# Kernel tuning notes

Hardware: AMD Instinct MI355X
Metric: run time of the kernel (lower is better)

## Reference

```python
import jax, jax.numpy as jnp
import numpy as np

EPS = 1e-5

def layer_norm(x, g, b):
    mu = jnp.mean(x, axis=-1, keepdims=True)
    var = jnp.var(x, axis=-1, keepdims=True)
    return (x - mu) * jax.lax.rsqrt(var + EPS) * g + b

def setup_inputs() -> dict:
    key = jax.random.key(0)
    ks = jax.random.split(key, 8)
    B, N, C, H = 4, 1024, 1024, 16
    Dh = C * 4
    std = 0.02
    return {
        "x": jax.random.normal(ks[0], (B, N, C), dtype=jnp.float32),
        "qkv_w": jax.random.normal(ks[1], (3 * C, C), dtype=jnp.float32) * std,
        "proj_w": jax.random.normal(ks[2], (C, C), dtype=jnp.float32) * std,
        "proj_b": jnp.zeros((C,), dtype=jnp.float32),
        "fc1_w": jax.random.normal(ks[3], (Dh, C), dtype=jnp.float32) * std,
        "fc1_b": jnp.zeros((Dh,), dtype=jnp.float32),
        "fc2_w": jax.random.normal(ks[4], (C, Dh), dtype=jnp.float32) * std,
        "fc2_b": jnp.zeros((C,), dtype=jnp.float32),
        "ln1_g": jnp.ones((C,), dtype=jnp.float32),
        "ln1_b": jnp.zeros((C,), dtype=jnp.float32),
        "ln2_g": jnp.ones((C,), dtype=jnp.float32),
        "ln2_b": jnp.zeros((C,), dtype=jnp.float32),
        "lnh_g": jnp.ones((Dh,), dtype=jnp.float32),
        "lnh_b": jnp.zeros((Dh,), dtype=jnp.float32),
    }

def reference(x, qkv_w, proj_w, proj_b, fc1_w, fc1_b, fc2_w, fc2_b,
              ln1_g, ln1_b, ln2_g, ln2_b, lnh_g, lnh_b):
    B, N, C = x.shape
    H = 16
    Dh = C // H
    scale = Dh ** (-0.5)

    # --- attention sublayer (pre-norm) ---
    h = layer_norm(x, ln1_g, ln1_b)
    qkv = (h @ qkv_w.T).reshape(B, N, 3, H, Dh).transpose(2, 0, 3, 1, 4)  # [3,B,H,N,Dh]
    q, k, v = qkv[0], qkv[1], qkv[2]
    attn = jnp.einsum('bhid,bhjd->bhij', q, k) * scale
    attn = jax.nn.softmax(attn, axis=-1)
    o = jnp.einsum('bhij,bhjd->bhid', attn, v)          # [B,H,N,Dh]
    o = o.transpose(0, 2, 1, 3).reshape(B, N, C)
    o = o @ proj_w.T + proj_b
    x = x + o

    # --- MLP sublayer (pre-norm, with LN on hidden per use_ln=True) ---
    h = layer_norm(x, ln2_g, ln2_b)
    u = jax.nn.gelu(h @ fc1_w.T + fc1_b, approximate=False)  # torch nn.GELU = erf form
    u = layer_norm(u, lnh_g, lnh_b)
    m = u @ fc2_w.T + fc2_b
    return x + m
```

## Files before the change

### kernel.cpp

```cpp
#include <hip/hip_runtime.h>
#include <hip/hip_bf16.h>
#include <math.h>


#define TOKENS 4096
#define CDIM   1024
#define HEADS  16
#define DHEAD  64
#define HID    4096

typedef __attribute__((ext_vector_type(4))) float  floatx4;
typedef __attribute__((ext_vector_type(8))) short  short8;

__device__ __forceinline__ void gl_lds16(const void* g, void* l)
{
    __builtin_amdgcn_global_load_lds(
        (const __attribute__((address_space(1))) unsigned int*)g,
        (__attribute__((address_space(3))) unsigned int*)l,
        16, 0, 0);
}

__global__ __launch_bounds__(256) void cvt_all(
    const float* __restrict__ s0, const float* __restrict__ s1,
    const float* __restrict__ s2, const float* __restrict__ s3,
    __hip_bfloat16* __restrict__ dst)
{
    long i = (long)blockIdx.x * 256 + threadIdx.x;
    const float* src;
    long base;
    if (i < 768l * 1024)       { src = s0; base = 0; }
    else if (i < 1792l * 1024) { src = s1; base = 768l * 1024; }
    else if (i < 2816l * 1024) { src = s2; base = 1792l * 1024; }
    else                       { src = s3; base = 2816l * 1024; }
    float4 v = ((const float4*)src)[i - base];
    __hip_bfloat16 t[4];
    t[0] = __float2bfloat16(v.x);
    t[1] = __float2bfloat16(v.y);
    t[2] = __float2bfloat16(v.z);
    t[3] = __float2bfloat16(v.w);
    *(uint2*)(dst + 4l * i) = *(uint2*)t;
}

__global__ __launch_bounds__(256) void ln_f32_kernel(
    const float* __restrict__ x, const float* __restrict__ g,
    const float* __restrict__ b, __hip_bfloat16* __restrict__ y, int C)
{
    int row = blockIdx.x;
    const float4* xr = (const float4*)(x + (long)row * C);
    uint2* yr = (uint2*)(y + (long)row * C);
    const int C4 = C >> 2;

    float s = 0.f, ss = 0.f;
    for (int i = threadIdx.x; i < C4; i += 256) {
        float4 v = xr[i];
        s  += v.x + v.y + v.z + v.w;
        ss += v.x * v.x + v.y * v.y + v.z * v.z + v.w * v.w;
    }
    #pragma unroll
    for (int d = 32; d; d >>= 1) {
        s  += __shfl_down(s, d);
        ss += __shfl_down(ss, d);
    }
    __shared__ float buf[4][2];
    int wid = threadIdx.x >> 6, lane = threadIdx.x & 63;
    if (lane == 0) { buf[wid][0] = s; buf[wid][1] = ss; }
    __syncthreads();
    if (threadIdx.x == 0) {
        s = buf[0][0] + buf[1][0] + buf[2][0] + buf[3][0];
        ss = buf[0][1] + buf[1][1] + buf[2][1] + buf[3][1];
        buf[0][0] = s; buf[0][1] = ss;
    }
    __syncthreads();
    s = buf[0][0]; ss = buf[0][1];

    float invC = 1.f / (float)C;
    float mu = s * invC;
    float var = ss * invC - mu * mu;
    float inv = rsqrtf(var + 1e-5f);
    const float4* gg = (const float4*)g;
    const float4* bb = (const float4*)b;
    for (int i = threadIdx.x; i < C4; i += 256) {
        float4 v = xr[i], gv = gg[i], bv = bb[i];
        __hip_bfloat16 t[4];
        t[0] = __float2bfloat16((v.x - mu) * inv * gv.x + bv.x);
        t[1] = __float2bfloat16((v.y - mu) * inv * gv.y + bv.y);
        t[2] = __float2bfloat16((v.z - mu) * inv * gv.z + bv.z);
        t[3] = __float2bfloat16((v.w - mu) * inv * gv.w + bv.w);
        yr[i] = *(uint2*)t;
    }
}

__global__ __launch_bounds__(256) void ln_bf16_kernel(
    const __hip_bfloat16* __restrict__ x, const float* __restrict__ g,
    const float* __restrict__ b, __hip_bfloat16* __restrict__ y, int C)
{
    int row = blockIdx.x;
    const uint4* xr = (const uint4*)(x + (long)row * C);
    uint4* yr = (uint4*)(y + (long)row * C);
    const int C8 = C >> 3;

    float s = 0.f, ss = 0.f;
    for (int i = threadIdx.x; i < C8; i += 256) {
        uint4 raw = xr[i];
        const __hip_bfloat16* p = (const __hip_bfloat16*)&raw;
        #pragma unroll
        for (int j = 0; j < 8; ++j) {
            float v = __bfloat162float(p[j]);
            s += v; ss += v * v;
        }
    }
    #pragma unroll
    for (int d = 32; d; d >>= 1) {
        s  += __shfl_down(s, d);
        ss += __shfl_down(ss, d);
    }
    __shared__ float buf[4][2];
    int wid = threadIdx.x >> 6, lane = threadIdx.x & 63;
    if (lane == 0) { buf[wid][0] = s; buf[wid][1] = ss; }
    __syncthreads();
    if (threadIdx.x == 0) {
        s = buf[0][0] + buf[1][0] + buf[2][0] + buf[3][0];
        ss = buf[0][1] + buf[1][1] + buf[2][1] + buf[3][1];
        buf[0][0] = s; buf[0][1] = ss;
    }
    __syncthreads();
    s = buf[0][0]; ss = buf[0][1];

    float invC = 1.f / (float)C;
    float mu = s * invC;
    float var = ss * invC - mu * mu;
    float inv = rsqrtf(var + 1e-5f);
    const float4* gg = (const float4*)g;
    const float4* bb = (const float4*)b;
    for (int i = threadIdx.x; i < C8; i += 256) {
        uint4 raw = xr[i];
        const __hip_bfloat16* p = (const __hip_bfloat16*)&raw;
        float4 g0 = gg[2 * i], g1 = gg[2 * i + 1];
        float4 b0 = bb[2 * i], b1 = bb[2 * i + 1];
        __hip_bfloat16 t[8];
        t[0] = __float2bfloat16((__bfloat162float(p[0]) - mu) * inv * g0.x + b0.x);
        t[1] = __float2bfloat16((__bfloat162float(p[1]) - mu) * inv * g0.y + b0.y);
        t[2] = __float2bfloat16((__bfloat162float(p[2]) - mu) * inv * g0.z + b0.z);
        t[3] = __float2bfloat16((__bfloat162float(p[3]) - mu) * inv * g0.w + b0.w);
        t[4] = __float2bfloat16((__bfloat162float(p[4]) - mu) * inv * g1.x + b1.x);
        t[5] = __float2bfloat16((__bfloat162float(p[5]) - mu) * inv * g1.y + b1.y);
        t[6] = __float2bfloat16((__bfloat162float(p[6]) - mu) * inv * g1.z + b1.z);
        t[7] = __float2bfloat16((__bfloat162float(p[7]) - mu) * inv * g1.w + b1.w);
        yr[i] = *(uint4*)t;
    }
}

__global__ __launch_bounds__(256, 3) void gemm_gl(
    const __hip_bfloat16* __restrict__ A,
    const __hip_bfloat16* __restrict__ W,
    const float* __restrict__ bias,
    void* __restrict__ Cout, int M, int N, int K, int mode)
{
    __shared__ __align__(16) __hip_bfloat16 Asl[128][64];
    __shared__ __align__(16) __hip_bfloat16 Bsl[128][64];

    int tid = threadIdx.x;
    int wave = tid >> 6, lane = tid & 63;

    int mt, nt;
    {
        int gx = gridDim.x, gy = gridDim.y;
        int lin = blockIdx.y * gx + blockIdx.x;
        int chunk = gy >> 3;
        int xcd = lin & 7, q = lin >> 3;
        mt = xcd * chunk + (q % chunk);
        nt = q / chunk;
    }
    int bm = mt * 128, bn = nt * 128;
    int wm = wave & 1, wn = wave >> 1;
    int fm = lane & 15, quad = lane >> 4;

    const int KS = K / gridDim.z;
    const long kz = (long)blockIdx.z * KS;
    const int nk = KS / 64;

    const int rsub = lane >> 3;
    const int csub = lane & 7;
    const __hip_bfloat16* gA[4];
    const __hip_bfloat16* gB[4];
    char* dA[4];
    char* dB[4];
    #pragma unroll
    for (int j = 0; j < 4; ++j) {
        int seg = wave * 4 + j;
        gA[j] = A + (long)(bm + seg * 8 + rsub) * K + kz + csub * 8;
        gB[j] = W + (long)(bn + seg * 8 + rsub) * K + kz + csub * 8;
        dA[j] = (char*)&Asl[0][0] + seg * 1024;
        dB[j] = (char*)&Bsl[0][0] + seg * 1024;
    }

    floatx4 acc[4][4] = {};

    for (int kt = 0; kt < nk; ++kt) {
        const long ko = (long)kt * 64;
        #pragma unroll
        for (int j = 0; j < 4; ++j) {
            gl_lds16(gA[j] + ko, dA[j]);
            gl_lds16(gB[j] + ko, dB[j]);
        }
        __syncthreads();

        #pragma unroll
        for (int kh = 0; kh < 2; ++kh) {
            short8 bq[4];
            #pragma unroll
            for (int j = 0; j < 4; ++j)
                bq[j] = *(const short8*)((const char*)&Bsl[0][0]
                        + (wn * 64 + j * 16 + fm) * 128 + kh * 64 + quad * 16);
            #pragma unroll
            for (int i = 0; i < 4; ++i) {
                short8 af = *(const short8*)((const char*)&Asl[0][0]
                        + (wm * 64 + i * 16 + fm) * 128 + kh * 64 + quad * 16);
                #pragma unroll
                for (int j = 0; j < 4; ++j)
                    acc[i][j] = __builtin_amdgcn_mfma_f32_16x16x32_bf16(
                        af, bq[j], acc[i][j], 0, 0, 0);
            }
        }
        __syncthreads();
    }

    int mbase = bm + wm * 64;
    int nbase = bn + wn * 64;
    if (mode == 2) {
        float* Cf = (float*)Cout;
        const bool addb = (blockIdx.z == 0);
        #pragma unroll
        for (int i = 0; i < 4; ++i) {
            #pragma unroll
            for (int j = 0; j < 4; ++j) {
                int ncol = nbase + j * 16 + fm;
                float bv = addb ? bias[ncol] : 0.f;
                #pragma unroll
                for (int r = 0; r < 4; ++r) {
                    int mrow = mbase + i * 16 + quad * 4 + r;
                    atomicAdd(&Cf[(long)mrow * N + ncol], acc[i][j][r] + bv);
                }
            }
        }
    } else {
        __hip_bfloat16* Cb = (__hip_bfloat16*)Cout;
        #pragma unroll
        for (int i = 0; i < 4; ++i) {
            #pragma unroll
            for (int j = 0; j < 4; ++j) {
                int ncol = nbase + j * 16 + fm;
                #pragma unroll
                for (int r = 0; r < 4; ++r) {
                    int mrow = mbase + i * 16 + quad * 4 + r;
                    float v = acc[i][j][r];
                    if (bias) v += bias[ncol];
                    if (mode == 1) {
                        float z = v * (1.5957691216f + 0.0713548162f * v * v);
                        v = v / (1.f + __expf(-z));
                    }
                    Cb[(long)mrow * N + ncol] = __float2bfloat16(v);
                }
            }
        }
    }
}

#define STR128 80
__global__ __launch_bounds__(256, 3) void gemm128res(
    const __hip_bfloat16* __restrict__ A,
    const __hip_bfloat16* __restrict__ W,
    const float* __restrict__ bias, const float* __restrict__ residual,
    float* __restrict__ Cout, int M, int N, int K)
{
    __shared__ __align__(16) char Asl[2][128 * STR128];
    __shared__ __align__(16) char Bsl[2][128 * STR128];

    int tid = threadIdx.x;
    int wave = tid >> 6, lane = tid & 63;

    int mt, nt;
    {
        int gx = gridDim.x, gy = gridDim.y;
        int lin = blockIdx.y * gx + blockIdx.x;
        int chunk = gy >> 3;
        int xcd = lin & 7, q = lin >> 3;
        mt = xcd * chunk + (q % chunk);
        nt = q / chunk;
    }
    int bm = mt * 128, bn = nt * 128;
    int wm = wave & 1, wn = wave >> 1;
    int fm = lane & 15, quad = lane >> 4;

    int srow = lane >> 2;
    int skb  = (lane & 3) * 16;

    const __hip_bfloat16* Ap = A + (long)(bm + wave * 16 + srow) * K + (lane & 3) * 8;
    const __hip_bfloat16* Bp = W + (long)(bn + wave * 16 + srow) * K + (lane & 3) * 8;
    const long a64 = (long)64 * K;

    const int nk = K / 32;
    floatx4 acc[4][4] = {};
    const int aoff = (wave * 16 + srow) * STR128 + skb;

    uint4 a0 = *(const uint4*)(Ap);
    uint4 a1 = *(const uint4*)(Ap + a64);
    uint4 b0 = *(const uint4*)(Bp);
    uint4 b1 = *(const uint4*)(Bp + a64);

    *(uint4*)(Asl[0] + aoff) = a0;
    *(uint4*)(Asl[0] + aoff + 64 * STR128) = a1;
    *(uint4*)(Bsl[0] + aoff) = b0;
    *(uint4*)(Bsl[0] + aoff + 64 * STR128) = b1;

    a0 = *(const uint4*)(Ap + 32);
    a1 = *(const uint4*)(Ap + a64 + 32);
    b0 = *(const uint4*)(Bp + 32);
    b1 = *(const uint4*)(Bp + a64 + 32);

    __syncthreads();

    for (int kt = 0; kt < nk; ++kt) {
        const int buf = kt & 1;
        const char* Ab = Asl[buf];
        const char* Bb = Bsl[buf];

        short8 bfr[4];
        #pragma unroll
        for (int j = 0; j < 4; ++j)
            bfr[j] = *(const short8*)(Bb + (wn * 64 + j * 16 + fm) * STR128 + quad * 16);
        #pragma unroll
        for (int i = 0; i < 4; ++i) {
            short8 af = *(const short8*)(Ab + (wm * 64 + i * 16 + fm) * STR128 + quad * 16);
            #pragma unroll
            for (int j = 0; j < 4; ++j)
                acc[i][j] = __builtin_amdgcn_mfma_f32_16x16x32_bf16(
                    af, bfr[j], acc[i][j], 0, 0, 0);
        }

        if (kt + 1 < nk) {
            const int nb = buf ^ 1;
            *(uint4*)(Asl[nb] + aoff) = a0;
            *(uint4*)(Asl[nb] + aoff + 64 * STR128) = a1;
            *(uint4*)(Bsl[nb] + aoff) = b0;
            *(uint4*)(Bsl[nb] + aoff + 64 * STR128) = b1;
            if (kt + 2 < nk) {
                const long o = (long)(kt + 2) * 32;
                a0 = *(const uint4*)(Ap + o);
                a1 = *(const uint4*)(Ap + a64 + o);
                b0 = *(const uint4*)(Bp + o);
                b1 = *(const uint4*)(Bp + a64 + o);
            }
        }
        __syncthreads();
    }

    int mbase = bm + wm * 64;
    int nbase = bn + wn * 64;
    #pragma unroll
    for (int i = 0; i < 4; ++i) {
        #pragma unroll
        for (int j = 0; j < 4; ++j) {
            int ncol = nbase + j * 16 + fm;
            float bv = bias[ncol];
            #pragma unroll
            for (int r = 0; r < 4; ++r) {
                int mrow = mbase + i * 16 + quad * 4 + r;
                long idx = (long)mrow * N + ncol;
                Cout[idx] = acc[i][j][r] + bv + residual[idx];
            }
        }
    }
}

__global__ __launch_bounds__(256) void attn_mfma(
    const __hip_bfloat16* __restrict__ qkv, __hip_bfloat16* __restrict__ o_out)
{
    __shared__ __align__(16) char Ks[2][64 * 144];
    __shared__ __align__(16) char Vt[2][64 * 144];
    __shared__ __align__(16) char Ps[4 * 16 * 144];

    const int C3 = 3 * CDIM;
    int lin = blockIdx.x;
    int xcd = lin & 7, q = lin >> 3;
    int bh = xcd * 8 + (q >> 4);
    int qt = q & 15;
    int b = bh >> 4, hh = bh & 15;
    int tid = threadIdx.x, wave = tid >> 6, lane = tid & 63;
    int l = lane & 15, quad = lane >> 4;

    const __hip_bfloat16* qrow =
        qkv + (long)(b * 1024 + qt * 64 + wave * 16 + l) * C3 + hh * DHEAD;
    short8 qf0 = *(const short8*)(qrow + quad * 8);
    short8 qf1 = *(const short8*)(qrow + 32 + quad * 8);

    char* Psw = Ps + wave * (16 * 144);

    int sc = tid & 7;
    int skl = tid >> 3;

    const __hip_bfloat16* Kbase = qkv + (long)(b * 1024) * C3 + CDIM + hh * DHEAD;
    const __hip_bfloat16* Vbase = qkv + (long)(b * 1024) * C3 + 2 * CDIM + hh * DHEAD;
    const int kpp = skl ^ (sc << 2);

    floatx4 facc[4] = {};
    float mrun = -1e30f, lrun = 0.f;

    uint4 kA0, kA1, vA0, vA1;
    uint4 kB0, kB1, vB0, vB1;

#define GKV(t, k0, k1, v0, v1) { \
    const __hip_bfloat16* Kg = Kbase + (long)((t) * 64) * C3; \
    const __hip_bfloat16* Vg = Vbase + (long)((t) * 64) * C3; \
    k0 = *(const uint4*)(Kg + (long)skl * C3 + sc * 8); \
    k1 = *(const uint4*)(Kg + (long)(skl + 32) * C3 + sc * 8); \
    v0 = *(const uint4*)(Vg + (long)(2 * skl) * C3 + sc * 8); \
    v1 = *(const uint4*)(Vg + (long)(2 * skl + 1) * C3 + sc * 8); }
#define WKV(bf, k0, k1, v0, v1) { \
    *(uint4*)(Ks[bf] + skl * 144 + sc * 16) = k0; \
    *(uint4*)(Ks[bf] + (skl + 32) * 144 + sc * 16) = k1; \
    const ushort* e0 = (const ushort*)&v0; \
    const ushort* e1 = (const ushort*)&v1; \
    _Pragma("unroll") \
    for (int j = 0; j < 8; ++j) { \
        unsigned dw = (unsigned)e0[j] | ((unsigned)e1[j] << 16); \
        *(unsigned*)(Vt[bf] + (sc * 8 + j) * 144 + kpp * 4) = dw; \
    } }

    auto compute = [&](int buf) {
        floatx4 st[4] = {};
        #pragma unroll
        for (int kb = 0; kb < 4; ++kb) {
            short8 k0 = *(const short8*)(Ks[buf] + (kb * 16 + l) * 144 + quad * 16);
            short8 k1 = *(const short8*)(Ks[buf] + (kb * 16 + l) * 144 + 64 + quad * 16);
            st[kb] = __builtin_amdgcn_mfma_f32_16x16x32_bf16(k0, qf0, st[kb], 0, 0, 0);
            st[kb] = __builtin_amdgcn_mfma_f32_16x16x32_bf16(k1, qf1, st[kb], 0, 0, 0);
        }
        float p[16];
        float tm = -1e30f;
        #pragma unroll
        for (int kb = 0; kb < 4; ++kb)
            #pragma unroll
            for (int r = 0; r < 4; ++r) {
                float s = st[kb][r] * 0.125f;
                p[kb * 4 + r] = s;
                tm = fmaxf(tm, s);
            }
        tm = fmaxf(tm, __shfl_xor(tm, 16));
        tm = fmaxf(tm, __shfl_xor(tm, 32));
        float mn = fmaxf(mrun, tm);
        float alpha = __expf(mrun - mn);
        float psum = 0.f;
        #pragma unroll
        for (int i = 0; i < 16; ++i) { p[i] = __expf(p[i] - mn); psum += p[i]; }
        psum += __shfl_xor(psum, 16);
        psum += __shfl_xor(psum, 32);
        lrun = lrun * alpha + psum;
        mrun = mn;

        #pragma unroll
        for (int kb = 0; kb < 4; ++kb) {
            __hip_bfloat16 t[4];
            #pragma unroll
            for (int r = 0; r < 4; ++r) t[r] = __float2bfloat16(p[kb * 4 + r]);
            *(uint2*)(Psw + l * 144 + kb * 32 + quad * 8) = *(const uint2*)t;
        }

        float a0 = __shfl(alpha, quad * 4 + 0);
        float a1 = __shfl(alpha, quad * 4 + 1);
        float a2 = __shfl(alpha, quad * 4 + 2);
        float a3 = __shfl(alpha, quad * 4 + 3);
        #pragma unroll
        for (int db = 0; db < 4; ++db) {
            facc[db][0] *= a0; facc[db][1] *= a1;
            facc[db][2] *= a2; facc[db][3] *= a3;
        }

        short8 pf0 = *(const short8*)(Psw + l * 144 + quad * 16);
        short8 pf1 = *(const short8*)(Psw + l * 144 + 64 + quad * 16);
        #pragma unroll
        for (int db = 0; db < 4; ++db) {
            int d = db * 16 + l;
            int o3 = (d >> 3) & 7;
            short8 v0 = *(const short8*)(Vt[buf] + d * 144 + ((quad ^ o3) << 4));
            short8 v1 = *(const short8*)(Vt[buf] + d * 144 + (((4 + quad) ^ o3) << 4));
            facc[db] = __builtin_amdgcn_mfma_f32_16x16x32_bf16(pf0, v0, facc[db], 0, 0, 0);
            facc[db] = __builtin_amdgcn_mfma_f32_16x16x32_bf16(pf1, v1, facc[db], 0, 0, 0);
        }
    };

    GKV(0, kA0, kA1, vA0, vA1);
    #pragma unroll 1
    for (int kt = 0; kt < 16; kt += 2) {
        WKV(0, kA0, kA1, vA0, vA1);
        __syncthreads();
        GKV(kt + 1, kB0, kB1, vB0, vB1);
        compute(0);
        WKV(1, kB0, kB1, vB0, vB1);
        __syncthreads();
        if (kt + 2 < 16) GKV(kt + 2, kA0, kA1, vA0, vA1);
        compute(1);
    }
#undef GKV
#undef WKV

    float il0 = 1.f / __shfl(lrun, quad * 4 + 0);
    float il1 = 1.f / __shfl(lrun, quad * 4 + 1);
    float il2 = 1.f / __shfl(lrun, quad * 4 + 2);
    float il3 = 1.f / __shfl(lrun, quad * 4 + 3);
    __hip_bfloat16* orow =
        o_out + (long)(b * 1024 + qt * 64 + wave * 16) * CDIM + hh * DHEAD;
    #pragma unroll
    for (int db = 0; db < 4; ++db) {
        int col = db * 16 + l;
        orow[(quad * 4 + 0) * CDIM + col] = __float2bfloat16(facc[db][0] * il0);
        orow[(quad * 4 + 1) * CDIM + col] = __float2bfloat16(facc[db][1] * il1);
        orow[(quad * 4 + 2) * CDIM + col] = __float2bfloat16(facc[db][2] * il2);
        orow[(quad * 4 + 3) * CDIM + col] = __float2bfloat16(facc[db][3] * il3);
    }
}

extern "C" void kernel_launch(void* const* d_in, const int* in_sizes, int n_in,
                              void* d_out, int out_size, void* d_ws, size_t ws_size,
                              hipStream_t stream)
{
    const float* x      = (const float*)d_in[0];
    const float* qkv_w  = (const float*)d_in[1];
    const float* proj_w = (const float*)d_in[2];
    const float* proj_b = (const float*)d_in[3];
    const float* fc1_w  = (const float*)d_in[4];
    const float* fc1_b  = (const float*)d_in[5];
    const float* fc2_w  = (const float*)d_in[6];
    const float* fc2_b  = (const float*)d_in[7];
    const float* ln1_g  = (const float*)d_in[8];
    const float* ln1_b  = (const float*)d_in[9];
    const float* ln2_g  = (const float*)d_in[10];
    const float* ln2_b  = (const float*)d_in[11];
    const float* lnh_g  = (const float*)d_in[12];
    const float* lnh_b  = (const float*)d_in[13];

    float* out = (float*)d_out;

    __hip_bfloat16* wsb     = (__hip_bfloat16*)d_ws;
    __hip_bfloat16* qkvw_bf = wsb;
    __hip_bfloat16* fc1w_bf = qkvw_bf + 3l * 1024 * 1024;
    __hip_bfloat16* fc2w_bf = fc1w_bf + 4l * 1024 * 1024;
    __hip_bfloat16* projw_bf= fc2w_bf + 4l * 1024 * 1024;
    __hip_bfloat16* h_bf    = projw_bf + 1l * 1024 * 1024;
    __hip_bfloat16* qkv_bf  = h_bf + 4l * 1024 * 1024;
    __hip_bfloat16* o_bf    = qkv_bf + 12l * 1024 * 1024;
    __hip_bfloat16* u_bf    = o_bf + 4l * 1024 * 1024;

    cvt_all<<<12288, 256, 0, stream>>>(qkv_w, fc1_w, fc2_w, proj_w, qkvw_bf);

    ln_f32_kernel<<<TOKENS, 256, 0, stream>>>(x, ln1_g, ln1_b, h_bf, CDIM);
    gemm_gl<<<dim3(3072 / 128, TOKENS / 128, 1), 256, 0, stream>>>(
        h_bf, qkvw_bf, nullptr, qkv_bf, TOKENS, 3072, CDIM, 0);
    attn_mfma<<<1024, 256, 0, stream>>>(qkv_bf, o_bf);
    gemm128res<<<dim3(CDIM / 128, TOKENS / 128), 256, 0, stream>>>(
        o_bf, projw_bf, proj_b, x, out, TOKENS, CDIM, CDIM);
    ln_f32_kernel<<<TOKENS, 256, 0, stream>>>(out, ln2_g, ln2_b, h_bf, CDIM);
    gemm_gl<<<dim3(HID / 128, TOKENS / 128, 1), 256, 0, stream>>>(
        h_bf, fc1w_bf, fc1_b, u_bf, TOKENS, HID, CDIM, 1);
    ln_bf16_kernel<<<TOKENS, 256, 0, stream>>>(u_bf, lnh_g, lnh_b, u_bf, HID);
    gemm_gl<<<dim3(CDIM / 128, TOKENS / 128, 4), 256, 0, stream>>>(
        u_bf, fc2w_bf, fc2_b, out, TOKENS, CDIM, HID, 2);
}
```

Baseline: 381.7 us.

## Unify GEMMs into double-buffered swizzled LDS kernel, drop split-K atomics

Replaces the single-buffered global-to-LDS GEMM and the separate register-staged projection GEMM with one kernel. The new kernel double-buffers LDS so the next K tile's async load overlaps the current MFMA work, and XOR-swizzles the LDS column layout to avoid bank conflicts. The fc2 GEMM drops its split-K atomicAdd and does a plain store with the residual added in place. That removes atomic traffic but cuts fc2 to 256 blocks with a K=4096 loop, and occupancy hints fall from 3 to 2 blocks per CU.

```diff
diff --git a/kernel.cpp b/kernel.cpp
--- a/kernel.cpp
+++ b/kernel.cpp
@@ -150,14 +150,14 @@
     }
 }
 
-__global__ __launch_bounds__(256, 3) void gemm_gl(
+__global__ __launch_bounds__(256, 2) void gemm_db(
     const __hip_bfloat16* __restrict__ A,
     const __hip_bfloat16* __restrict__ W,
-    const float* __restrict__ bias,
+    const float* __restrict__ bias, const float* __restrict__ residual,
     void* __restrict__ Cout, int M, int N, int K, int mode)
 {
-    __shared__ __align__(16) __hip_bfloat16 Asl[128][64];
-    __shared__ __align__(16) __hip_bfloat16 Bsl[128][64];
+    __shared__ __align__(16) char Asl[2][16384];
+    __shared__ __align__(16) char Bsl[2][16384];
 
     int tid = threadIdx.x;
     int wave = tid >> 6, lane = tid & 63;
@@ -174,48 +174,52 @@
     int bm = mt * 128, bn = nt * 128;
     int wm = wave & 1, wn = wave >> 1;
     int fm = lane & 15, quad = lane >> 4;
-
-    const int KS = K / gridDim.z;
-    const long kz = (long)blockIdx.z * KS;
-    const int nk = KS / 64;
+    const int r7 = fm & 7;
+
+    const int nk = K / 64;
 
     const int rsub = lane >> 3;
-    const int csub = lane & 7;
+    const int csub = (lane & 7) ^ rsub;
     const __hip_bfloat16* gA[4];
     const __hip_bfloat16* gB[4];
-    char* dA[4];
-    char* dB[4];
+    int dseg[4];
     #pragma unroll
     for (int j = 0; j < 4; ++j) {
         int seg = wave * 4 + j;
-        gA[j] = A + (long)(bm + seg * 8 + rsub) * K + kz + csub * 8;
-        gB[j] = W + (long)(bn + seg * 8 + rsub) * K + kz + csub * 8;
-        dA[j] = (char*)&Asl[0][0] + seg * 1024;
-        dB[j] = (char*)&Bsl[0][0] + seg * 1024;
-    }
+        gA[j] = A + (long)(bm + seg * 8 + rsub) * K + csub * 8;
+        gB[j] = W + (long)(bn + seg * 8 + rsub) * K + csub * 8;
+        dseg[j] = seg * 1024;
+    }
+
+#define STAGE(b, kt) { \
+    const long ko = (long)(kt) * 64; \
+    _Pragma("unroll") \
+    for (int j = 0; j < 4; ++j) { \
+        gl_lds16(gA[j] + ko, Asl[b] + dseg[j]); \
+        gl_lds16(gB[j] + ko, Bsl[b] + dseg[j]); \
+    } }
 
     floatx4 acc[4][4] = {};
 
+    STAGE(0, 0);
+    __syncthreads();
+
+    int cur = 0;
     for (int kt = 0; kt < nk; ++kt) {
-        const long ko = (long)kt * 64;
-        #pragma unroll
-        for (int j = 0; j < 4; ++j) {
-            gl_lds16(gA[j] + ko, dA[j]);
-            gl_lds16(gB[j] + ko, dB[j]);
-        }
-        __syncthreads();
-
+        if (kt + 1 < nk) STAGE(cur ^ 1, kt + 1);
+
+        const char* Ab = Asl[cur];
+        const char* Bb = Bsl[cur];
         #pragma unroll
         for (int kh = 0; kh < 2; ++kh) {
+            const int xsw = ((kh * 4 + quad) ^ r7) << 4;
             short8 bq[4];
             #pragma unroll
             for (int j = 0; j < 4; ++j)
-                bq[j] = *(const short8*)((const char*)&Bsl[0][0]
-                        + (wn * 64 + j * 16 + fm) * 128 + kh * 64 + quad * 16);
+                bq[j] = *(const short8*)(Bb + (wn * 64 + j * 16 + fm) * 128 + xsw);
             #pragma unroll
             for (int i = 0; i < 4; ++i) {
-                short8 af = *(const short8*)((const char*)&Asl[0][0]
-                        + (wm * 64 + i * 16 + fm) * 128 + kh * 64 + quad * 16);
+                short8 af = *(const short8*)(Ab + (wm * 64 + i * 16 + fm) * 128 + xsw);
                 #pragma unroll
                 for (int j = 0; j < 4; ++j)
                     acc[i][j] = __builtin_amdgcn_mfma_f32_16x16x32_bf16(
@@ -223,23 +227,25 @@
             }
         }
         __syncthreads();
-    }
+        cur ^= 1;
+    }
+#undef STAGE
 
     int mbase = bm + wm * 64;
     int nbase = bn + wn * 64;
     if (mode == 2) {
         float* Cf = (float*)Cout;
-        const bool addb = (blockIdx.z == 0);
         #pragma unroll
         for (int i = 0; i < 4; ++i) {
             #pragma unroll
             for (int j = 0; j < 4; ++j) {
                 int ncol = nbase + j * 16 + fm;
-                float bv = addb ? bias[ncol] : 0.f;
+                float bv = bias[ncol];
                 #pragma unroll
                 for (int r = 0; r < 4; ++r) {
                     int mrow = mbase + i * 16 + quad * 4 + r;
-                    atomicAdd(&Cf[(long)mrow * N + ncol], acc[i][j][r] + bv);
+                    long idx = (long)mrow * N + ncol;
+                    Cf[idx] = acc[i][j][r] + bv + residual[idx];
                 }
             }
         }
@@ -261,113 +267,6 @@
                     }
                     Cb[(long)mrow * N + ncol] = __float2bfloat16(v);
                 }
-            }
-        }
-    }
-}
-
-#define STR128 80
-__global__ __launch_bounds__(256, 3) void gemm128res(
-    const __hip_bfloat16* __restrict__ A,
-    const __hip_bfloat16* __restrict__ W,
-    const float* __restrict__ bias, const float* __restrict__ residual,
-    float* __restrict__ Cout, int M, int N, int K)
-{
-    __shared__ __align__(16) char Asl[2][128 * STR128];
-    __shared__ __align__(16) char Bsl[2][128 * STR128];
-
-    int tid = threadIdx.x;
-    int wave = tid >> 6, lane = tid & 63;
-
-    int mt, nt;
-    {
-        int gx = gridDim.x, gy = gridDim.y;
-        int lin = blockIdx.y * gx + blockIdx.x;
-        int chunk = gy >> 3;
-        int xcd = lin & 7, q = lin >> 3;
-        mt = xcd * chunk + (q % chunk);
-        nt = q / chunk;
-    }
-    int bm = mt * 128, bn = nt * 128;
-    int wm = wave & 1, wn = wave >> 1;
-    int fm = lane & 15, quad = lane >> 4;
-
-    int srow = lane >> 2;
-    int skb  = (lane & 3) * 16;
-
-    const __hip_bfloat16* Ap = A + (long)(bm + wave * 16 + srow) * K + (lane & 3) * 8;
-    const __hip_bfloat16* Bp = W + (long)(bn + wave * 16 + srow) * K + (lane & 3) * 8;
-    const long a64 = (long)64 * K;
-
-    const int nk = K / 32;
-    floatx4 acc[4][4] = {};
-    const int aoff = (wave * 16 + srow) * STR128 + skb;
-
-    uint4 a0 = *(const uint4*)(Ap);
-    uint4 a1 = *(const uint4*)(Ap + a64);
-    uint4 b0 = *(const uint4*)(Bp);
-    uint4 b1 = *(const uint4*)(Bp + a64);
-
-    *(uint4*)(Asl[0] + aoff) = a0;
-    *(uint4*)(Asl[0] + aoff + 64 * STR128) = a1;
-    *(uint4*)(Bsl[0] + aoff) = b0;
-    *(uint4*)(Bsl[0] + aoff + 64 * STR128) = b1;
-
-    a0 = *(const uint4*)(Ap + 32);
-    a1 = *(const uint4*)(Ap + a64 + 32);
-    b0 = *(const uint4*)(Bp + 32);
-    b1 = *(const uint4*)(Bp + a64 + 32);
-
-    __syncthreads();
-
-    for (int kt = 0; kt < nk; ++kt) {
-        const int buf = kt & 1;
-        const char* Ab = Asl[buf];
-        const char* Bb = Bsl[buf];
-
-        short8 bfr[4];
-        #pragma unroll
-        for (int j = 0; j < 4; ++j)
-            bfr[j] = *(const short8*)(Bb + (wn * 64 + j * 16 + fm) * STR128 + quad * 16);
-        #pragma unroll
-        for (int i = 0; i < 4; ++i) {
-            short8 af = *(const short8*)(Ab + (wm * 64 + i * 16 + fm) * STR128 + quad * 16);
-            #pragma unroll
-            for (int j = 0; j < 4; ++j)
-                acc[i][j] = __builtin_amdgcn_mfma_f32_16x16x32_bf16(
-                    af, bfr[j], acc[i][j], 0, 0, 0);
-        }
-
-        if (kt + 1 < nk) {
-            const int nb = buf ^ 1;
-            *(uint4*)(Asl[nb] + aoff) = a0;
-            *(uint4*)(Asl[nb] + aoff + 64 * STR128) = a1;
-            *(uint4*)(Bsl[nb] + aoff) = b0;
-            *(uint4*)(Bsl[nb] + aoff + 64 * STR128) = b1;
-            if (kt + 2 < nk) {
-                const long o = (long)(kt + 2) * 32;
-                a0 = *(const uint4*)(Ap + o);
-                a1 = *(const uint4*)(Ap + a64 + o);
-                b0 = *(const uint4*)(Bp + o);
-                b1 = *(const uint4*)(Bp + a64 + o);
-            }
-        }
-        __syncthreads();
-    }
-
-    int mbase = bm + wm * 64;
-    int nbase = bn + wn * 64;
-    #pragma unroll
-    for (int i = 0; i < 4; ++i) {
-        #pragma unroll
-        for (int j = 0; j < 4; ++j) {
-            int ncol = nbase + j * 16 + fm;
-            float bv = bias[ncol];
-            #pragma unroll
-            for (int r = 0; r < 4; ++r) {
-                int mrow = mbase + i * 16 + quad * 4 + r;
-                long idx = (long)mrow * N + ncol;
-                Cout[idx] = acc[i][j][r] + bv + residual[idx];
             }
         }
     }
@@ -554,15 +453,15 @@
     cvt_all<<<12288, 256, 0, stream>>>(qkv_w, fc1_w, fc2_w, proj_w, qkvw_bf);
 
     ln_f32_kernel<<<TOKENS, 256, 0, stream>>>(x, ln1_g, ln1_b, h_bf, CDIM);
-    gemm_gl<<<dim3(3072 / 128, TOKENS / 128, 1), 256, 0, stream>>>(
-        h_bf, qkvw_bf, nullptr, qkv_bf, TOKENS, 3072, CDIM, 0);
+    gemm_db<<<dim3(3072 / 128, TOKENS / 128), 256, 0, stream>>>(
+        h_bf, qkvw_bf, nullptr, nullptr, qkv_bf, TOKENS, 3072, CDIM, 0);
     attn_mfma<<<1024, 256, 0, stream>>>(qkv_bf, o_bf);
-    gemm128res<<<dim3(CDIM / 128, TOKENS / 128), 256, 0, stream>>>(
-        o_bf, projw_bf, proj_b, x, out, TOKENS, CDIM, CDIM);
+    gemm_db<<<dim3(CDIM / 128, TOKENS / 128), 256, 0, stream>>>(
+        o_bf, projw_bf, proj_b, x, out, TOKENS, CDIM, CDIM, 2);
     ln_f32_kernel<<<TOKENS, 256, 0, stream>>>(out, ln2_g, ln2_b, h_bf, CDIM);
-    gemm_gl<<<dim3(HID / 128, TOKENS / 128, 1), 256, 0, stream>>>(
-        h_bf, fc1w_bf, fc1_b, u_bf, TOKENS, HID, CDIM, 1);
+    gemm_db<<<dim3(HID / 128, TOKENS / 128), 256, 0, stream>>>(
+        h_bf, fc1w_bf, fc1_b, nullptr, u_bf, TOKENS, HID, CDIM, 1);
     ln_bf16_kernel<<<TOKENS, 256, 0, stream>>>(u_bf, lnh_g, lnh_b, u_bf, HID);
-    gemm_gl<<<dim3(CDIM / 128, TOKENS / 128, 4), 256, 0, stream>>>(
-        u_bf, fc2w_bf, fc2_b, out, TOKENS, CDIM, HID, 2);
-}
+    gemm_db<<<dim3(CDIM / 128, TOKENS / 128), 256, 0, stream>>>(
+        u_bf, fc2w_bf, fc2_b, out, out, TOKENS, CDIM, HID, 2);
+}
```

After: 386.7 us. Within noise of the previous version (+1.3%).
